# Performance work log

Hardware: AMD Instinct MI355X
Metric: run time of the kernel (lower is better)

## Reference

```python
import jax, jax.numpy as jnp
import numpy as np

N = 50000      # total nodes
E = 500000     # edges
D = 128        # in_channels
B = 50         # graphs in batch
NPG = N // B   # nodes per graph (equal-sized graphs)
RATIO = 0.5
ALPHA = 0.6


def setup_inputs() -> dict:
    key = jax.random.key(0)
    ks = jax.random.split(key, 8)
    x = jax.random.normal(ks[0], (N, D), dtype=jnp.float32)
    edge_index = jax.random.randint(ks[1], (2, E), 0, N, dtype=jnp.int32)
    batch = jnp.repeat(jnp.arange(B, dtype=jnp.int32), NPG)  # sorted, equal blocks
    s = 1.0 / np.sqrt(D)
    # GCNConv(D,1) for structure score
    W_s = jax.random.normal(ks[2], (D, 1), dtype=jnp.float32) * s
    b_s = jnp.zeros((1,), dtype=jnp.float32)
    # Linear(D,1) for feature score
    W_f = jax.random.normal(ks[3], (1, D), dtype=jnp.float32) * s
    b_f = jnp.zeros((1,), dtype=jnp.float32)
    # GCNConv(D,D) fusion layer
    W_fu = jax.random.normal(ks[4], (D, D), dtype=jnp.float32) * s
    b_fu = jnp.zeros((D,), dtype=jnp.float32)
    return {"x": x, "edge_index": edge_index, "batch": batch,
            "W_s": W_s, "b_s": b_s, "W_f": W_f, "b_f": b_f,
            "W_fu": W_fu, "b_fu": b_fu}


def gcn_conv(x, src, dst, W, b, n):
    """PyG GCNConv: add self loops, symmetric D^-1/2 (A+I) D^-1/2 @ (xW) + b."""
    xw = x @ W                                  # [n, out]
    loop = jnp.arange(n, dtype=src.dtype)
    s = jnp.concatenate([src, loop])
    d = jnp.concatenate([dst, loop])
    deg = jax.ops.segment_sum(jnp.ones_like(s, dtype=xw.dtype), d, num_segments=n)
    dinv = jax.lax.rsqrt(jnp.maximum(deg, 1e-12))
    norm = dinv[s] * dinv[d]                    # [E+n]
    out = jax.ops.segment_sum(norm[:, None] * xw[s], d, num_segments=n)
    return out + b


def reference(x, edge_index, batch, W_s, b_s, W_f, b_f, W_fu, b_fu):
    src, dst = edge_index[0], edge_index[1]
    # fused score: alpha * structure (GCN) + (1-alpha) * feature (Linear)
    score_s = gcn_conv(x, src, dst, W_s, b_s, N)[:, 0]          # [N]
    score_f = (x @ W_f.T + b_f)[:, 0]                           # [N]
    score = jnp.tanh(ALPHA * score_s + (1.0 - ALPHA) * score_f)
    # per-graph top-k (equal-sized graphs -> dense [B, NPG] view, like the torch topk)
    k = int(np.ceil(RATIO * NPG))
    dense = score.reshape(B, NPG)
    order = jnp.argsort(-dense, axis=-1)                        # descending
    offsets = (jnp.arange(B, dtype=jnp.int32) * NPG)[:, None]
    perm = (order[:, :k].astype(jnp.int32) + offsets).reshape(-1)  # [B*k]
    # fusion conv on full graph, then gather selected nodes
    x_fused = gcn_conv(x, src, dst, W_fu, b_fu, N)              # [N, D]
    x_ae = x_fused[perm]                                        # [B*k, D]
    x_out = x_ae * score[perm][:, None]                         # multiplier == 1
    batch_out = batch[perm]
    # filter_adj: remap node ids, keep edges with both endpoints selected
    nodemap = jnp.full((N,), -1, dtype=jnp.int32).at[perm].set(
        jnp.arange(perm.shape[0], dtype=jnp.int32))
    r, c = nodemap[src], nodemap[dst]
    m = (r >= 0) & (c >= 0)
    edge_index_new = jnp.stack([r[m], c[m]], axis=0)
    return (x_out, edge_index_new, batch_out, perm, x_ae)
```

## Files before the change

kernel.cpp:

```cpp
#include <hip/hip_runtime.h>
#include <math.h>

#define N_NODES 50000
#define N_EDGES 500000
#define DIM     128
#define NGRAPH  50
#define NPGC    1000
#define KSEL    500
#define SORT_N  1024
#define NBE     489
#define NBN     49
#define GEMM_BLKS 782
#define DEG_BLKS  1954
#define DOTS_BLKS 12500
#define NDINV     196
#define GATH_BLKS 6250


__global__ __launch_bounds__(256) void k1_gemm_deg(const float* __restrict__ x,
                                                   const float* __restrict__ W,
                                                   float* __restrict__ xw,
                                                   const int* __restrict__ dst,
                                                   int* __restrict__ deg) {
    __shared__ float lds[12288];
    int t = threadIdx.x;
    if (blockIdx.x >= GEMM_BLKS) {
        int e = (blockIdx.x - GEMM_BLKS) * 256 + t;
        if (e < N_EDGES) atomicAdd(&deg[dst[e]], 1);
        return;
    }
    float* Wt = lds;
    float* Xt = lds + 64 * DIM;
    int cg = t & 15;
    int ng = t >> 4;
    int node_base = blockIdx.x * 64;

    float4 acc[4][2];
    #pragma unroll
    for (int nn = 0; nn < 4; nn++) {
        acc[nn][0] = make_float4(0.f, 0.f, 0.f, 0.f);
        acc[nn][1] = make_float4(0.f, 0.f, 0.f, 0.f);
    }
    for (int half = 0; half < 2; half++) {
        const float4* Wg = (const float4*)(W + half * 64 * DIM);
        float4* Wl = (float4*)Wt;
        #pragma unroll
        for (int i = 0; i < 8; i++) {
            int f = t + i * 256;
            Wl[f] = Wg[f];
        }
        #pragma unroll
        for (int i = 0; i < 4; i++) {
            int f = t + i * 256;
            int row = f >> 4, col = f & 15;
            int node = node_base + row;
            float4 v = make_float4(0.f, 0.f, 0.f, 0.f);
            if (node < N_NODES) v = *(const float4*)&x[(size_t)node * DIM + half * 64 + col * 4];
            *(float4*)&Xt[(row << 6) + ((col ^ (row & 15)) << 2)] = v;
        }
        __syncthreads();
        #pragma unroll 2
        for (int kc = 0; kc < 16; kc++) {
            int k = kc << 2;
            float4 wa[4], wb[4];
            #pragma unroll
            for (int kk = 0; kk < 4; kk++) {
                wa[kk] = *(const float4*)&Wt[(k + kk) * DIM + (cg << 2)];
                wb[kk] = *(const float4*)&Wt[(k + kk) * DIM + (cg << 2) + 64];
            }
            int csw = (kc ^ ng) << 2;
            #pragma unroll
            for (int nn = 0; nn < 4; nn++) {
                float4 xv = *(const float4*)&Xt[((ng + (nn << 4)) << 6) + csw];
                acc[nn][0].x += xv.x * wa[0].x + xv.y * wa[1].x + xv.z * wa[2].x + xv.w * wa[3].x;
                acc[nn][0].y += xv.x * wa[0].y + xv.y * wa[1].y + xv.z * wa[2].y + xv.w * wa[3].y;
                acc[nn][0].z += xv.x * wa[0].z + xv.y * wa[1].z + xv.z * wa[2].z + xv.w * wa[3].z;
                acc[nn][0].w += xv.x * wa[0].w + xv.y * wa[1].w + xv.z * wa[2].w + xv.w * wa[3].w;
                acc[nn][1].x += xv.x * wb[0].x + xv.y * wb[1].x + xv.z * wb[2].x + xv.w * wb[3].x;
                acc[nn][1].y += xv.x * wb[0].y + xv.y * wb[1].y + xv.z * wb[2].y + xv.w * wb[3].y;
                acc[nn][1].z += xv.x * wb[0].z + xv.y * wb[1].z + xv.z * wb[2].z + xv.w * wb[3].z;
                acc[nn][1].w += xv.x * wb[0].w + xv.y * wb[1].w + xv.z * wb[2].w + xv.w * wb[3].w;
            }
        }
        __syncthreads();
    }
    #pragma unroll
    for (int nn = 0; nn < 4; nn++) {
        int node = node_base + ng + (nn << 4);
        if (node < N_NODES) {
            *(float4*)&xw[(size_t)node * DIM + (cg << 2)]      = acc[nn][0];
            *(float4*)&xw[(size_t)node * DIM + (cg << 2) + 64] = acc[nn][1];
        }
    }
}


__global__ __launch_bounds__(256) void k2_dots_scan_dinv(const int* __restrict__ deg,
                                                         int* __restrict__ rowoff,
                                                         int* __restrict__ bsumsN,
                                                         const float* __restrict__ x,
                                                         const float* __restrict__ Ws,
                                                         const float* __restrict__ Wf,
                                                         const float* __restrict__ bf,
                                                         double* __restrict__ pack,
                                                         float* __restrict__ dinvf,
                                                         double* __restrict__ sf) {
    int t = threadIdx.x;
    int lane = t & 63, wid = t >> 6;
    int bid = blockIdx.x;
    if (bid < DOTS_BLKS) {
        int node = bid * 4 + wid;
        const float* xr = x + (size_t)node * DIM;
        double x1 = (double)xr[lane], x2 = (double)xr[lane + 64];
        double ps = x1 * (double)Ws[lane] + x2 * (double)Ws[lane + 64];
        double pf = x1 * (double)Wf[lane] + x2 * (double)Wf[lane + 64];
        for (int off = 32; off > 0; off >>= 1) {
            ps += __shfl_down(ps, off, 64);
            pf += __shfl_down(pf, off, 64);
        }
        if (lane == 0) {
            pack[2 * node + 1] = ps;
            sf[node] = pf + (double)bf[0];
        }
        return;
    }
    if (bid < DOTS_BLKS + NBN) {
        __shared__ int ws4[4];
        int base = (bid - DOTS_BLKS) * 1024 + t * 4;
        int v0 = (base + 0 < N_NODES) ? deg[base + 0] : 0;
        int v1 = (base + 1 < N_NODES) ? deg[base + 1] : 0;
        int v2 = (base + 2 < N_NODES) ? deg[base + 2] : 0;
        int v3 = (base + 3 < N_NODES) ? deg[base + 3] : 0;
        int s4 = v0 + v1 + v2 + v3;
        int incl = s4;
        #pragma unroll
        for (int off = 1; off < 64; off <<= 1) {
            int u = __shfl_up(incl, off, 64);
            if (lane >= off) incl += u;
        }
        if (lane == 63) ws4[wid] = incl;
        __syncthreads();
        int woff = 0;
        #pragma unroll
        for (int w = 0; w < 4; w++) if (w < wid) woff += ws4[w];
        int excl = incl - s4 + woff;
        if (base + 0 < N_NODES) rowoff[base + 0] = excl;
        if (base + 1 < N_NODES) rowoff[base + 1] = excl + v0;
        if (base + 2 < N_NODES) rowoff[base + 2] = excl + v0 + v1;
        if (base + 3 < N_NODES) rowoff[base + 3] = excl + v0 + v1 + v2;
        if (t == 255) bsumsN[bid - DOTS_BLKS] = woff + incl;
        return;
    }
    int i = (bid - DOTS_BLKS - NBN) * 256 + t;
    if (i < N_NODES) {
        double di = 1.0 / sqrt((double)(deg[i] + 1));
        pack[2 * i] = di;
        dinvf[i] = (float)di;
    }
}


__global__ __launch_bounds__(256) void k3_csr(const int* __restrict__ src,
                                              const int* __restrict__ dst,
                                              const int* __restrict__ rowoff,
                                              const int* __restrict__ bsumsN,
                                              int* __restrict__ cursor,
                                              int* __restrict__ csr) {
    __shared__ int bsN[64];
    int t = threadIdx.x;
    if (t < 64) {
        int v = (t < NBN) ? bsumsN[t] : 0;
        int incl = v;
        #pragma unroll
        for (int off = 1; off < 64; off <<= 1) {
            int u = __shfl_up(incl, off, 64);
            if (t >= off) incl += u;
        }
        bsN[t] = incl - v;
    }
    __syncthreads();
    int e = blockIdx.x * 256 + t;
    if (e >= N_EDGES) return;
    int d = dst[e];
    int pos = rowoff[d] + bsN[d >> 10] + atomicAdd(&cursor[d], 1);
    csr[pos] = src[e];
}


__global__ __launch_bounds__(1024) void k4_topk(const int* __restrict__ csr,
                                                const int* __restrict__ rowoff,
                                                const int* __restrict__ bsumsN,
                                                const int* __restrict__ deg,
                                                const double* __restrict__ pack,
                                                const double* __restrict__ sf,
                                                const float* __restrict__ bs,
                                                int* __restrict__ perm, int* __restrict__ nodemap,
                                                float* __restrict__ scoref_sel,
                                                float* __restrict__ out, long o2, long o3) {
    __shared__ double key[SORT_N];
    __shared__ int    idx[SORT_N];
    __shared__ int    bsN[64];
    int g = blockIdx.x, t = threadIdx.x;
    if (t < 64) {
        int v = (t < NBN) ? bsumsN[t] : 0;
        int incl = v;
        #pragma unroll
        for (int off = 1; off < 64; off <<= 1) {
            int u = __shfl_up(incl, off, 64);
            if (t >= off) incl += u;
        }
        bsN[t] = incl - v;
    }
    __syncthreads();
    const double A = 0.6, OMA = 1.0 - 0.6;
    double bsv = (double)bs[0];
    {
        int i = t;
        if (i < NPGC) {
            int node = g * NPGC + i;
            int base = rowoff[node] + bsN[node >> 10];
            int cnt  = deg[node];
            double acc0 = 0.0, acc1 = 0.0;
            int e = 0;
            for (; e + 2 <= cnt; e += 2) {
                int s0 = csr[base + e];
                int s1 = csr[base + e + 1];
                double2 p0 = ((const double2*)pack)[s0];
                double2 p1 = ((const double2*)pack)[s1];
                acc0 += p0.x * p0.y;
                acc1 += p1.x * p1.y;
            }
            if (e < cnt) {
                int s0 = csr[base + e];
                double2 p0 = ((const double2*)pack)[s0];
                acc0 += p0.x * p0.y;
            }
            double2 pn = ((const double2*)pack)[node];
            double tot = pn.x * (acc0 + acc1) + pn.x * pn.x * pn.y + bsv;
            key[i] = tanh(A * tot + OMA * sf[node]);
            idx[i] = i;
        } else if (i < SORT_N) { key[i] = -1e300; idx[i] = i; }
    }
    __syncthreads();
    for (int size = 2; size <= SORT_N; size <<= 1) {
        for (int stride = size >> 1; stride > 0; stride >>= 1) {
            if (t < 512) {
                int a = ((t & ~(stride - 1)) << 1) | (t & (stride - 1));
                int b = a | stride;
                bool descFirst = ((a & size) == 0);
                double ka = key[a], kb = key[b];
                int ia = idx[a], ib = idx[b];
                bool aAfterB = (ka < kb) || (ka == kb && ia > ib);
                if (descFirst ? aAfterB : !aAfterB) {
                    key[a] = kb; key[b] = ka;
                    idx[a] = ib; idx[b] = ia;
                }
            }
            __syncthreads();
        }
    }
    if (t < KSEL) {
        int j = t;
        int node = g * NPGC + idx[j];
        int pos  = g * KSEL + j;
        perm[pos]        = node;
        nodemap[node]    = pos + 1;
        scoref_sel[pos]  = (float)key[j];
        out[o2 + pos]    = (float)g;
        out[o3 + pos]    = (float)node;
    }
}


__global__ __launch_bounds__(256) void k5_escan_gather(const int* __restrict__ src,
                                                       const int* __restrict__ dst,
                                                       const int* __restrict__ nodemap,
                                                       int* __restrict__ epos,
                                                       int* __restrict__ bsumsE,
                                                       const float* __restrict__ xw,
                                                       const int* __restrict__ perm,
                                                       const int* __restrict__ rowoff,
                                                       const int* __restrict__ bsumsN,
                                                       const int* __restrict__ deg,
                                                       const int* __restrict__ csr,
                                                       const float* __restrict__ dinvf,
                                                       const float* __restrict__ scoref_sel,
                                                       const float* __restrict__ b_fu,
                                                       float* __restrict__ out, long o4) {
    int t = threadIdx.x;
    int lane = t & 63, wid = t >> 6;
    if (blockIdx.x < NBE) {
        __shared__ int ws4[4];
        int base = blockIdx.x * 1024 + t * 4;
        int v0 = 0, v1 = 0, v2 = 0, v3 = 0;
        if (base + 0 < N_EDGES) v0 = (nodemap[src[base + 0]] > 0 && nodemap[dst[base + 0]] > 0);
        if (base + 1 < N_EDGES) v1 = (nodemap[src[base + 1]] > 0 && nodemap[dst[base + 1]] > 0);
        if (base + 2 < N_EDGES) v2 = (nodemap[src[base + 2]] > 0 && nodemap[dst[base + 2]] > 0);
        if (base + 3 < N_EDGES) v3 = (nodemap[src[base + 3]] > 0 && nodemap[dst[base + 3]] > 0);
        int s4 = v0 + v1 + v2 + v3;
        int incl = s4;
        #pragma unroll
        for (int off = 1; off < 64; off <<= 1) {
            int u = __shfl_up(incl, off, 64);
            if (lane >= off) incl += u;
        }
        if (lane == 63) ws4[wid] = incl;
        __syncthreads();
        int woff = 0;
        #pragma unroll
        for (int w = 0; w < 4; w++) if (w < wid) woff += ws4[w];
        int excl = incl - s4 + woff;
        if (base + 0 < N_EDGES) epos[base + 0] = excl;
        if (base + 1 < N_EDGES) epos[base + 1] = excl + v0;
        if (base + 2 < N_EDGES) epos[base + 2] = excl + v0 + v1;
        if (base + 3 < N_EDGES) epos[base + 3] = excl + v0 + v1 + v2;
        if (t == 255) bsumsE[blockIdx.x] = woff + incl;
        return;
    }
    __shared__ int bsN[64];
    if (t < 64) {
        int v = (t < NBN) ? bsumsN[t] : 0;
        int incl = v;
        #pragma unroll
        for (int off = 1; off < 64; off <<= 1) {
            int u = __shfl_up(incl, off, 64);
            if (t >= off) incl += u;
        }
        bsN[t] = incl - v;
    }
    __syncthreads();
    int wave = (blockIdx.x - NBE) * 4 + wid;
    int p = perm[wave];
    float dpf = dinvf[p];
    int c2 = lane * 2;
    float2 v = ((const float2*)(xw + (size_t)p * DIM))[lane];
    float nself = dpf * dpf;
    float ax = nself * v.x, ay = nself * v.y;
    int beg = rowoff[p] + bsN[p >> 10], cnt = deg[p];
    int i = 0;
    for (; i + 2 <= cnt; i += 2) {
        int s0 = csr[beg + i];
        int s1 = csr[beg + i + 1];
        float2 u0 = ((const float2*)(xw + (size_t)s0 * DIM))[lane];
        float2 u1 = ((const float2*)(xw + (size_t)s1 * DIM))[lane];
        float n0 = dinvf[s0] * dpf, n1 = dinvf[s1] * dpf;
        ax += n0 * u0.x; ay += n0 * u0.y;
        ax += n1 * u1.x; ay += n1 * u1.y;
    }
    if (i < cnt) {
        int s0 = csr[beg + i];
        float2 u0 = ((const float2*)(xw + (size_t)s0 * DIM))[lane];
        float n0 = dinvf[s0] * dpf;
        ax += n0 * u0.x; ay += n0 * u0.y;
    }
    ax += b_fu[c2];
    ay += b_fu[c2 + 1];
    float sc = scoref_sel[wave];
    size_t ro = (size_t)wave * DIM + c2;
    out[o4 + ro]     = ax;
    out[o4 + ro + 1] = ay;
    out[ro]          = ax * sc;
    out[ro + 1]      = ay * sc;
}


__global__ __launch_bounds__(256) void k6_compact(const int* __restrict__ src,
                                                  const int* __restrict__ dst,
                                                  const int* __restrict__ nodemap,
                                                  const int* __restrict__ epos,
                                                  const int* __restrict__ bsumsE,
                                                  float* __restrict__ out_edges, long M) {
    __shared__ int bsE[512];
    int t = threadIdx.x;
    if (t < 64) {
        int carry = 0;
        #pragma unroll
        for (int c = 0; c < 8; c++) {
            int i = c * 64 + t;
            int v = (i < NBE) ? bsumsE[i] : 0;
            int incl = v;
            #pragma unroll
            for (int off = 1; off < 64; off <<= 1) {
                int u = __shfl_up(incl, off, 64);
                if (t >= off) incl += u;
            }
            if (i < 512) bsE[i] = incl - v + carry;
            carry += __shfl(incl, 63, 64);
        }
    }
    __syncthreads();
    int e = blockIdx.x * 256 + t;
    if (e >= N_EDGES) return;
    int r = nodemap[src[e]], c = nodemap[dst[e]];
    if (r > 0 && c > 0) {
        int pos = epos[e] + bsE[e >> 10];
        out_edges[pos]     = (float)(r - 1);
        out_edges[M + pos] = (float)(c - 1);
    }
}


extern "C" void kernel_launch(void* const* d_in, const int* in_sizes, int n_in,
                              void* d_out, int out_size, void* d_ws, size_t ws_size,
                              hipStream_t stream) {
    const float* x    = (const float*)d_in[0];
    const int*   ei   = (const int*)d_in[1];
    const int*   src  = ei;
    const int*   dst  = ei + N_EDGES;
    const float* W_s  = (const float*)d_in[3];
    const float* b_s  = (const float*)d_in[4];
    const float* W_f  = (const float*)d_in[5];
    const float* b_f  = (const float*)d_in[6];
    const float* W_fu = (const float*)d_in[7];
    const float* b_fu = (const float*)d_in[8];
    float* out = (float*)d_out;

    char* wsp = (char*)d_ws;
    size_t off = 0;
    auto take = [&](size_t bytes) -> char* {
        char* p = wsp + off;
        off = (off + bytes + 255) & ~(size_t)255;
        return p;
    };
    char*   zbase      = wsp;
    int*    deg        = (int*)   take((size_t)N_NODES * 4);
    int*    cursor     = (int*)   take((size_t)N_NODES * 4);
    int*    nodemap    = (int*)   take((size_t)N_NODES * 4);
    size_t  zbytes     = off;
    double* pack       = (double*)take((size_t)N_NODES * 16);
    double* sf         = (double*)take((size_t)N_NODES * 8);
    float*  dinvf      = (float*) take((size_t)N_NODES * 4);
    float*  scoref_sel = (float*) take((size_t)NGRAPH * KSEL * 4);
    int*    perm       = (int*)   take((size_t)NGRAPH * KSEL * 4);
    int*    rowoff     = (int*)   take((size_t)N_NODES * 4);
    int*    epos       = (int*)   take((size_t)N_EDGES * 4);
    int*    bsumsE     = (int*)   take((size_t)1024 * 4);
    int*    bsumsN     = (int*)   take((size_t)1024 * 4);
    int*    csr        = (int*)   take((size_t)N_EDGES * 4);
    float*  xw         = (float*) take((size_t)N_NODES * DIM * 4);

    long M  = ((long)out_size - 6450000L) / 2;
    long o1 = 3200000L;
    long o2 = o1 + 2 * M;
    long o3 = o2 + (long)NGRAPH * KSEL;
    long o4 = o3 + (long)NGRAPH * KSEL;

    hipMemsetAsync(zbase, 0, zbytes, stream);

    k1_gemm_deg<<<GEMM_BLKS + DEG_BLKS, 256, 0, stream>>>(x, W_fu, xw, dst, deg);
    k2_dots_scan_dinv<<<DOTS_BLKS + NBN + NDINV, 256, 0, stream>>>(deg, rowoff, bsumsN,
                                                                   x, W_s, W_f, b_f,
                                                                   pack, dinvf, sf);
    k3_csr<<<DEG_BLKS, 256, 0, stream>>>(src, dst, rowoff, bsumsN, cursor, csr);
    k4_topk<<<NGRAPH, 1024, 0, stream>>>(csr, rowoff, bsumsN, deg, pack, sf, b_s,
                                         perm, nodemap, scoref_sel, out, o2, o3);
    k5_escan_gather<<<NBE + GATH_BLKS, 256, 0, stream>>>(src, dst, nodemap, epos, bsumsE,
                                                         xw, perm, rowoff, bsumsN, deg, csr,
                                                         dinvf, scoref_sel, b_fu, out, o4);
    k6_compact<<<DEG_BLKS, 256, 0, stream>>>(src, dst, nodemap, epos, bsumsE, out + o1, M);
}
```

Measured before the change: 240.2 us.

## Compute x@W_fu with split-bf16 MFMA instead of FP32 FMA

Replaces the scalar FP32 FMA GEMM in the fused gemm/degree kernel with MFMA 16x16x32 bf16 instructions. Both operands are split into bf16 high and low parts, and three MFMAs (hh, hl, lh) approximate FP32 accuracy. A small prep kernel converts W into swizzled bf16 hi/lo layouts, and x is split on the fly into LDS. This moves the 50000x128x128 GEMM onto the matrix cores, at the cost of an extra launch, conversion work and a slight loss of precision from dropping the lo*lo term.

```diff
diff --git a/kernel.cpp b/kernel.cpp
--- a/kernel.cpp
+++ b/kernel.cpp
@@ -16,80 +16,113 @@
 #define NDINV     196
 #define GATH_BLKS 6250
 
+typedef short s16x8 __attribute__((ext_vector_type(8)));
+typedef float f32x4 __attribute__((ext_vector_type(4)));
+
+__device__ __forceinline__ void f2bf2(float v, unsigned short& h, unsigned short& l) {
+    unsigned u = __float_as_uint(v);
+    unsigned hb = (u + 0x7FFFu + ((u >> 16) & 1u)) >> 16;
+    h = (unsigned short)hb;
+    float r = v - __uint_as_float(hb << 16);
+    unsigned u2 = __float_as_uint(r);
+    l = (unsigned short)((u2 + 0x7FFFu + ((u2 >> 16) & 1u)) >> 16);
+}
+
+
+__global__ __launch_bounds__(256) void k0_wprep(const float* __restrict__ W,
+                                                unsigned short* __restrict__ Wth,
+                                                unsigned short* __restrict__ Wtl) {
+    int idx = blockIdx.x * 256 + threadIdx.x;
+    int k = idx >> 7, ch = idx & 127;
+    unsigned short h, l;
+    f2bf2(W[idx], h, l);
+    int hh = k >> 6, kl = k & 63;
+    int pos = hh * 8192 + ch * 64 + ((((kl >> 3) ^ (ch & 7))) << 3) + (kl & 7);
+    Wth[pos] = h;
+    Wtl[pos] = l;
+}
+
 
 __global__ __launch_bounds__(256) void k1_gemm_deg(const float* __restrict__ x,
-                                                   const float* __restrict__ W,
+                                                   const unsigned short* __restrict__ Wth,
+                                                   const unsigned short* __restrict__ Wtl,
                                                    float* __restrict__ xw,
                                                    const int* __restrict__ dst,
                                                    int* __restrict__ deg) {
-    __shared__ float lds[12288];
+    __shared__ unsigned short lds_sh[24576];
     int t = threadIdx.x;
     if (blockIdx.x >= GEMM_BLKS) {
         int e = (blockIdx.x - GEMM_BLKS) * 256 + t;
         if (e < N_EDGES) atomicAdd(&deg[dst[e]], 1);
         return;
     }
-    float* Wt = lds;
-    float* Xt = lds + 64 * DIM;
-    int cg = t & 15;
-    int ng = t >> 4;
+    unsigned short* XH = lds_sh;
+    unsigned short* XL = lds_sh + 4096;
+    unsigned short* WH = lds_sh + 8192;
+    unsigned short* WL = lds_sh + 16384;
+    const int wv = t >> 6, lane = t & 63;
+    const int q = lane >> 4, mm = lane & 15;
     int node_base = blockIdx.x * 64;
 
-    float4 acc[4][2];
+    f32x4 zero4v = {0.f, 0.f, 0.f, 0.f};
+    f32x4 acc[8];
     #pragma unroll
-    for (int nn = 0; nn < 4; nn++) {
-        acc[nn][0] = make_float4(0.f, 0.f, 0.f, 0.f);
-        acc[nn][1] = make_float4(0.f, 0.f, 0.f, 0.f);
-    }
-    for (int half = 0; half < 2; half++) {
-        const float4* Wg = (const float4*)(W + half * 64 * DIM);
-        float4* Wl = (float4*)Wt;
-        #pragma unroll
-        for (int i = 0; i < 8; i++) {
-            int f = t + i * 256;
-            Wl[f] = Wg[f];
+    for (int ct = 0; ct < 8; ct++) acc[ct] = zero4v;
+
+    for (int h = 0; h < 2; h++) {
+        {
+            const s16x8* GH = (const s16x8*)(Wth + h * 8192);
+            const s16x8* GL = (const s16x8*)(Wtl + h * 8192);
+            s16x8* LH = (s16x8*)WH;
+            s16x8* LL = (s16x8*)WL;
+            #pragma unroll
+            for (int i = 0; i < 4; i++) {
+                LH[t + i * 256] = GH[t + i * 256];
+                LL[t + i * 256] = GL[t + i * 256];
+            }
         }
         #pragma unroll
         for (int i = 0; i < 4; i++) {
             int f = t + i * 256;
-            int row = f >> 4, col = f & 15;
-            int node = node_base + row;
+            int r = f >> 4, c4 = f & 15;
+            int node = node_base + r;
             float4 v = make_float4(0.f, 0.f, 0.f, 0.f);
-            if (node < N_NODES) v = *(const float4*)&x[(size_t)node * DIM + half * 64 + col * 4];
-            *(float4*)&Xt[(row << 6) + ((col ^ (row & 15)) << 2)] = v;
+            if (node < N_NODES) v = *(const float4*)&x[(size_t)node * DIM + h * 64 + c4 * 4];
+            unsigned short h0, l0, h1, l1, h2, l2, h3, l3;
+            f2bf2(v.x, h0, l0); f2bf2(v.y, h1, l1);
+            f2bf2(v.z, h2, l2); f2bf2(v.w, h3, l3);
+            int off = r * 64 + ((((c4 >> 1) ^ (r & 7))) << 3) + ((c4 & 1) << 2);
+            *(uint2*)&XH[off] = make_uint2((unsigned)h0 | ((unsigned)h1 << 16),
+                                           (unsigned)h2 | ((unsigned)h3 << 16));
+            *(uint2*)&XL[off] = make_uint2((unsigned)l0 | ((unsigned)l1 << 16),
+                                           (unsigned)l2 | ((unsigned)l3 << 16));
         }
         __syncthreads();
-        #pragma unroll 2
-        for (int kc = 0; kc < 16; kc++) {
-            int k = kc << 2;
-            float4 wa[4], wb[4];
+        #pragma unroll
+        for (int c = 0; c < 2; c++) {
+            int jb = c * 4 + q;
+            int aoff = (wv * 16 + mm) * 64 + ((jb ^ (mm & 7)) << 3);
+            s16x8 ah = *(const s16x8*)&XH[aoff];
+            s16x8 al = *(const s16x8*)&XL[aoff];
             #pragma unroll
-            for (int kk = 0; kk < 4; kk++) {
-                wa[kk] = *(const float4*)&Wt[(k + kk) * DIM + (cg << 2)];
-                wb[kk] = *(const float4*)&Wt[(k + kk) * DIM + (cg << 2) + 64];
-            }
-            int csw = (kc ^ ng) << 2;
-            #pragma unroll
-            for (int nn = 0; nn < 4; nn++) {
-                float4 xv = *(const float4*)&Xt[((ng + (nn << 4)) << 6) + csw];
-                acc[nn][0].x += xv.x * wa[0].x + xv.y * wa[1].x + xv.z * wa[2].x + xv.w * wa[3].x;
-                acc[nn][0].y += xv.x * wa[0].y + xv.y * wa[1].y + xv.z * wa[2].y + xv.w * wa[3].y;
-                acc[nn][0].z += xv.x * wa[0].z + xv.y * wa[1].z + xv.z * wa[2].z + xv.w * wa[3].z;
-                acc[nn][0].w += xv.x * wa[0].w + xv.y * wa[1].w + xv.z * wa[2].w + xv.w * wa[3].w;
-                acc[nn][1].x += xv.x * wb[0].x + xv.y * wb[1].x + xv.z * wb[2].x + xv.w * wb[3].x;
-                acc[nn][1].y += xv.x * wb[0].y + xv.y * wb[1].y + xv.z * wb[2].y + xv.w * wb[3].y;
-                acc[nn][1].z += xv.x * wb[0].z + xv.y * wb[1].z + xv.z * wb[2].z + xv.w * wb[3].z;
-                acc[nn][1].w += xv.x * wb[0].w + xv.y * wb[1].w + xv.z * wb[2].w + xv.w * wb[3].w;
+            for (int ct = 0; ct < 8; ct++) {
+                int ch = ct * 16 + mm;
+                int boff = ch * 64 + ((jb ^ (ch & 7)) << 3);
+                s16x8 bh = *(const s16x8*)&WH[boff];
+                s16x8 bl = *(const s16x8*)&WL[boff];
+                acc[ct] = __builtin_amdgcn_mfma_f32_16x16x32_bf16(ah, bh, acc[ct], 0, 0, 0);
+                acc[ct] = __builtin_amdgcn_mfma_f32_16x16x32_bf16(ah, bl, acc[ct], 0, 0, 0);
+                acc[ct] = __builtin_amdgcn_mfma_f32_16x16x32_bf16(al, bh, acc[ct], 0, 0, 0);
             }
         }
         __syncthreads();
     }
     #pragma unroll
-    for (int nn = 0; nn < 4; nn++) {
-        int node = node_base + ng + (nn << 4);
-        if (node < N_NODES) {
-            *(float4*)&xw[(size_t)node * DIM + (cg << 2)]      = acc[nn][0];
-            *(float4*)&xw[(size_t)node * DIM + (cg << 2) + 64] = acc[nn][1];
+    for (int ct = 0; ct < 8; ct++) {
+        #pragma unroll
+        for (int r = 0; r < 4; r++) {
+            int node = node_base + wv * 16 + q * 4 + r;
+            if (node < N_NODES) xw[(size_t)node * DIM + ct * 16 + mm] = acc[ct][r];
         }
     }
 }
@@ -438,6 +471,8 @@
     int*    bsumsN     = (int*)   take((size_t)1024 * 4);
     int*    csr        = (int*)   take((size_t)N_EDGES * 4);
     float*  xw         = (float*) take((size_t)N_NODES * DIM * 4);
+    unsigned short* Wth = (unsigned short*)take((size_t)16384 * 2);
+    unsigned short* Wtl = (unsigned short*)take((size_t)16384 * 2);
 
     long M  = ((long)out_size - 6450000L) / 2;
     long o1 = 3200000L;
@@ -447,7 +482,8 @@
 
     hipMemsetAsync(zbase, 0, zbytes, stream);
 
-    k1_gemm_deg<<<GEMM_BLKS + DEG_BLKS, 256, 0, stream>>>(x, W_fu, xw, dst, deg);
+    k0_wprep<<<64, 256, 0, stream>>>(W_fu, Wth, Wtl);
+    k1_gemm_deg<<<GEMM_BLKS + DEG_BLKS, 256, 0, stream>>>(x, Wth, Wtl, xw, dst, deg);
     k2_dots_scan_dinv<<<DOTS_BLKS + NBN + NDINV, 256, 0, stream>>>(deg, rowoff, bsumsN,
                                                                    x, W_s, W_f, b_f,
                                                                    pack, dinvf, sf);
```

New measurement: 233.0 us. 1.03x faster.
